# Performance work log

Hardware: AMD Instinct MI355X
Metric: run time of the kernel (lower is better)

The kernel has to match this reference:

```python
import jax, jax.numpy as jnp
import numpy as np

B, S, IN, HID, NH, HD, R, WIN, TK = 2, 2048, 64, 512, 8, 64, 64, 5, 16
C1, C2, C3 = 171, 171, 170  # hidden_dim split across 3 conv branches (512 = 171+171+170)


def _conv(xc, w, b, pad):
    y = jax.lax.conv_general_dilated(xc, w, window_strides=(1,), padding=[(pad, pad)],
                                     dimension_numbers=('NCH', 'OIH', 'NCH'))
    return jax.nn.relu(y + b[None, :, None])


def setup_inputs():
    key = jax.random.key(0)
    ks = jax.random.split(key, 22)
    p = lambda k, sh: jax.random.normal(k, sh, jnp.float32) * 0.05
    return {
        'x': jax.random.normal(ks[0], (B, S, IN), jnp.float32),
        'conv1_w': p(ks[1], (C1, IN, 3)), 'conv1_b': p(ks[2], (C1,)),
        'conv2_w': p(ks[3], (C2, IN, 5)), 'conv2_b': p(ks[4], (C2,)),
        'conv3_w': p(ks[5], (C3, IN, 7)), 'conv3_b': p(ks[6], (C3,)),
        'Wq': p(ks[7], (HID, HID)), 'bq': p(ks[8], (HID,)),
        'Wk': p(ks[9], (HID, HID)), 'bk': p(ks[10], (HID,)),
        'Wv': p(ks[11], (HID, HID)), 'bv': p(ks[12], (HID,)),
        'Wkp': p(ks[13], (R, HD)), 'bkp': p(ks[14], (R,)),
        'Wvp': p(ks[15], (R, HD)), 'bvp': p(ks[16], (R,)),
        'Wo': p(ks[17], (HID, HID)), 'bo': p(ks[18], (HID,)),
        'ln_g': jnp.ones((HID,), jnp.float32), 'ln_b': jnp.zeros((HID,), jnp.float32),
    }


def reference(x, conv1_w, conv1_b, conv2_w, conv2_b, conv3_w, conv3_b,
              Wq, bq, Wk, bk, Wv, bv, Wkp, bkp, Wvp, bvp, Wo, bo, ln_g, ln_b):
    # multi-scale conv front-end
    xc = x.transpose(0, 2, 1)  # [B, IN, S]
    h = jnp.concatenate([_conv(xc, conv1_w, conv1_b, 1),
                         _conv(xc, conv2_w, conv2_b, 2),
                         _conv(xc, conv3_w, conv3_b, 3)], axis=1).transpose(0, 2, 1)  # [B,S,HID]

    def heads(W_, b_):
        return (h @ W_.T + b_).reshape(B, S, NH, HD).transpose(0, 2, 1, 3)  # [B,NH,S,HD]

    Q, K, V = heads(Wq, bq), heads(Wk, bk), heads(Wv, bv)
    Kp = K @ Wkp.T + bkp  # [B,NH,S,R]
    Vp = V @ Wvp.T + bvp

    # local sliding-window attention; -inf masking reproduces the per-t boundary slicing
    hw = WIN // 2
    idx = jnp.arange(S)[:, None] + jnp.arange(-hw, hw + 1)[None, :]
    valid = (idx >= 0) & (idx < S)
    idxc = jnp.clip(idx, 0, S - 1)
    Kw = K[:, :, idxc, :]
    Vw = V[:, :, idxc, :]
    ls = jnp.einsum('bhsd,bhswd->bhsw', Q, Kw) / jnp.sqrt(jnp.float32(HD))
    ls = jnp.where(valid[None, None], ls, -jnp.inf)
    local = jnp.einsum('bhsw,bhswd->bhsd', jax.nn.softmax(ls, axis=-1), Vw)

    # top-k low-rank global attention (HD == R required by original einsum)
    gs = jnp.einsum('bhqd,bhkd->bhqk', Q, Kp) / jnp.sqrt(jnp.float32(R))  # [B,NH,S,S]
    tv, ti = jax.lax.top_k(gs, TK)
    tw = jax.nn.softmax(tv, axis=-1)  # [B,NH,S,TK]
    bi = jnp.arange(B)[:, None, None, None]
    hi = jnp.arange(NH)[None, :, None, None]
    topV = Vp[bi, hi, ti]  # [B,NH,S,TK,R]
    sp = jnp.einsum('bhqk,bhqkr->bhqr', tw, topV)
    sp = sp @ Wvp.T + bvp  # extra value_proj applied to sparse output, as in original

    out = ((local + sp) * 0.5).transpose(0, 2, 1, 3).reshape(B, S, HID)
    out = out @ Wo.T + bo
    res = out + h
    mu = res.mean(-1, keepdims=True)
    var = ((res - mu) ** 2).mean(-1, keepdims=True)
    return (res - mu) / jnp.sqrt(var + 1e-5) * ln_g + ln_b
```

## Files before the change

### kernel.cpp

```cpp
#include <hip/hip_runtime.h>
#include <hip/hip_bf16.h>

#define BB 2
#define SS 2048
#define INC 64
#define HIDN 512
#define NHH 8
#define HDD 64
#define SP 2054

typedef __attribute__((ext_vector_type(8))) short bf16x8;
typedef __attribute__((ext_vector_type(4))) float f32x4;

__device__ __forceinline__ short f2bf(float f) {
  union { __hip_bfloat16 h; short s; } u;
  u.h = __float2bfloat16(f);
  return u.s;
}
__device__ __forceinline__ float bf2f(short s) {
  return __uint_as_float(((unsigned)(unsigned short)s) << 16);
}


__global__ __launch_bounds__(256) void prep_kernel(
    const float* __restrict__ x, const float* __restrict__ w1,
    const float* __restrict__ b1, const float* __restrict__ w2,
    const float* __restrict__ b2, const float* __restrict__ w3,
    const float* __restrict__ b3, const float* __restrict__ Wq,
    const float* __restrict__ Wk_, const float* __restrict__ Wv_,
    const float* __restrict__ bq, const float* __restrict__ bk_,
    const float* __restrict__ bv_, const float* __restrict__ Wo,
    const float* __restrict__ Wkp, const float* __restrict__ Wvp,
    const float* __restrict__ bvp, short* __restrict__ Wallbf,
    float* __restrict__ ball, short* __restrict__ Wobf,
    short* __restrict__ Wkpbf, short* __restrict__ W2bf,
    float* __restrict__ cvec, short* __restrict__ xbfp,
    short* __restrict__ Wcbf, float* __restrict__ bcat) {
  int i0 = blockIdx.x * 256 + threadIdx.x;
  int stride = gridDim.x * 256;
  for (int g = i0; g < 98304; g += stride) {
    int n = g >> 6;
    int k = (g & 63) << 3;
    const float* src;
    if (n < 512)       src = Wq  + (size_t)n * 512 + k;
    else if (n < 1024) src = Wk_ + (size_t)(n - 512) * 512 + k;
    else               src = Wv_ + (size_t)(n - 1024) * 512 + k;
    float4 f0 = *(const float4*)src;
    float4 f1 = *(const float4*)(src + 4);
    bf16x8 v;
    v[0] = f2bf(f0.x); v[1] = f2bf(f0.y); v[2] = f2bf(f0.z); v[3] = f2bf(f0.w);
    v[4] = f2bf(f1.x); v[5] = f2bf(f1.y); v[6] = f2bf(f1.z); v[7] = f2bf(f1.w);
    size_t off = (size_t)(n >> 6) * 32768 + (size_t)(k >> 5) * 2048 +
                 (size_t)((n & 63) >> 4) * 512 +
                 ((((k & 31) >> 3) * 16 + (n & 15)) << 3);
    *(bf16x8*)(Wallbf + off) = v;
  }
  for (int g = i0; g < 32768; g += stride) {
    int n = g >> 6;
    int k = (g & 63) << 3;
    const float* src = Wo + (size_t)n * 512 + k;
    float4 f0 = *(const float4*)src;
    float4 f1 = *(const float4*)(src + 4);
    bf16x8 v;
    v[0] = f2bf(f0.x); v[1] = f2bf(f0.y); v[2] = f2bf(f0.z); v[3] = f2bf(f0.w);
    v[4] = f2bf(f1.x); v[5] = f2bf(f1.y); v[6] = f2bf(f1.z); v[7] = f2bf(f1.w);
    size_t off = (size_t)(n >> 6) * 32768 + (size_t)(k >> 5) * 2048 +
                 (size_t)((n & 63) >> 4) * 512 +
                 ((((k & 31) >> 3) * 16 + (n & 15)) << 3);
    *(bf16x8*)(Wobf + off) = v;
  }
  for (int g = i0; g < BB * SP * 8; g += stride) {
    int row = g >> 3, c0 = (g & 7) << 3;
    int b = row / SP, pr = row - b * SP;
    int sg = pr - 3;
    bf16x8 v;
    if (sg >= 0 && sg < SS) {
      const float* src = x + ((size_t)(b * SS + sg) << 6) + c0;
      float4 f0 = *(const float4*)src;
      float4 f1 = *(const float4*)(src + 4);
      v[0] = f2bf(f0.x); v[1] = f2bf(f0.y); v[2] = f2bf(f0.z); v[3] = f2bf(f0.w);
      v[4] = f2bf(f1.x); v[5] = f2bf(f1.y); v[6] = f2bf(f1.z); v[7] = f2bf(f1.w);
    } else {
#pragma unroll
      for (int e = 0; e < 8; e++) v[e] = 0;
    }
    *(bf16x8*)(xbfp + ((size_t)row << 3 << 3) + c0) = v;
  }
  for (int g = i0; g < 28672; g += stride) {
    int c = g / 56;
    int rem = g - c * 56;
    int k = rem << 3;
    int t = k >> 6;
    int ci0 = k & 63;
    bf16x8 v;
#pragma unroll
    for (int e = 0; e < 8; e++) {
      int ci = ci0 + e;
      float val = 0.f;
      if (c < 171) {
        int kk = t - 2;
        if (kk >= 0 && kk < 3) val = w1[(c * 64 + ci) * 3 + kk];
      } else if (c < 342) {
        int kk = t - 1;
        if (kk >= 0 && kk < 5) val = w2[((c - 171) * 64 + ci) * 5 + kk];
      } else {
        val = w3[((c - 342) * 64 + ci) * 7 + t];
      }
      v[e] = f2bf(val);
    }
    size_t off = (size_t)(c >> 6) * 28672 + (size_t)(k >> 5) * 2048 +
                 (size_t)((c & 63) >> 4) * 512 +
                 ((((k & 31) >> 3) * 16 + (c & 15)) << 3);
    *(bf16x8*)(Wcbf + off) = v;
  }
  for (int idx = i0; idx < 4096; idx += stride) {
    Wkpbf[idx] = f2bf(Wkp[idx]);
    int j = idx >> 6, d = idx & 63;
    float s = 0.f;
#pragma unroll 8
    for (int i = 0; i < 64; i++) s += Wvp[j * 64 + i] * Wvp[i * 64 + d];
    W2bf[idx] = f2bf(s);
  }
  if (i0 < 1536) {
    float v;
    if (i0 < 512)       v = bq[i0];
    else if (i0 < 1024) v = bk_[i0 - 512];
    else                v = bv_[i0 - 1024];
    ball[i0] = v;
  }
  if (i0 < 512) {
    float v;
    if (i0 < 171)      v = b1[i0];
    else if (i0 < 342) v = b2[i0 - 171];
    else               v = b3[i0 - 342];
    bcat[i0] = v;
  }
  if (i0 < 64) {
    float s = bvp[i0];
#pragma unroll 8
    for (int i = 0; i < 64; i++) s += bvp[i] * Wvp[i0 * 64 + i];
    cvec[i0] = s;
  }
}

__global__ __launch_bounds__(256, 4) void gemm_conv(
    const short* __restrict__ xbfp, const short* __restrict__ Wcbf,
    const float* __restrict__ bcat, short* __restrict__ hbf) {
  int m0 = blockIdx.x * 128;
  int n0 = blockIdx.y * 64;
  int tid = threadIdx.x;
  int wvv = tid >> 6, lane = tid & 63;
  int quad = lane >> 4, l16 = lane & 15;
  int mw = m0 + wvv * 32;
  int r0 = mw + l16, r1 = r0 + 16;
  int b0 = r0 >> 11, s0 = r0 & 2047;
  int b1 = r1 >> 11, s1 = r1 & 2047;
  const short* ap0 = xbfp + (size_t)(b0 * SP + s0) * 64 + quad * 8;
  const short* ap1 = xbfp + (size_t)(b1 * SP + s1) * 64 + quad * 8;
  const short* bp = Wcbf + (size_t)(n0 >> 6) * 28672 + lane * 8;
  f32x4 acc[2][4] = {};
  bf16x8 cA0 = *(const bf16x8*)ap0;
  bf16x8 cA1 = *(const bf16x8*)ap1;
  bf16x8 cB0 = *(const bf16x8*)(bp + 0 * 512);
  bf16x8 cB1 = *(const bf16x8*)(bp + 1 * 512);
  bf16x8 cB2 = *(const bf16x8*)(bp + 2 * 512);
  bf16x8 cB3 = *(const bf16x8*)(bp + 3 * 512);
#pragma unroll 2
  for (int ks = 0; ks < 14; ks++) {
    int kn = (ks + 1 < 14 ? ks + 1 : 13);
    int offa = kn * 32;
    int offb = kn * 2048;
    bf16x8 nA0 = *(const bf16x8*)(ap0 + offa);
    bf16x8 nA1 = *(const bf16x8*)(ap1 + offa);
    bf16x8 nB0 = *(const bf16x8*)(bp + offb + 0 * 512);
    bf16x8 nB1 = *(const bf16x8*)(bp + offb + 1 * 512);
    bf16x8 nB2 = *(const bf16x8*)(bp + offb + 2 * 512);
    bf16x8 nB3 = *(const bf16x8*)(bp + offb + 3 * 512);
    acc[0][0] = __builtin_amdgcn_mfma_f32_16x16x32_bf16(cA0, cB0, acc[0][0], 0, 0, 0);
    acc[1][0] = __builtin_amdgcn_mfma_f32_16x16x32_bf16(cA1, cB0, acc[1][0], 0, 0, 0);
    acc[0][1] = __builtin_amdgcn_mfma_f32_16x16x32_bf16(cA0, cB1, acc[0][1], 0, 0, 0);
    acc[1][1] = __builtin_amdgcn_mfma_f32_16x16x32_bf16(cA1, cB1, acc[1][1], 0, 0, 0);
    acc[0][2] = __builtin_amdgcn_mfma_f32_16x16x32_bf16(cA0, cB2, acc[0][2], 0, 0, 0);
    acc[1][2] = __builtin_amdgcn_mfma_f32_16x16x32_bf16(cA1, cB2, acc[1][2], 0, 0, 0);
    acc[0][3] = __builtin_amdgcn_mfma_f32_16x16x32_bf16(cA0, cB3, acc[0][3], 0, 0, 0);
    acc[1][3] = __builtin_amdgcn_mfma_f32_16x16x32_bf16(cA1, cB3, acc[1][3], 0, 0, 0);
    cA0 = nA0; cA1 = nA1;
    cB0 = nB0; cB1 = nB1; cB2 = nB2; cB3 = nB3;
  }
#pragma unroll
  for (int mt = 0; mt < 2; mt++) {
#pragma unroll
    for (int r = 0; r < 4; r++) {
      int m = mw + mt * 16 + quad * 4 + r;
#pragma unroll
      for (int t = 0; t < 4; t++) {
        int n = n0 + t * 16 + l16;
        float v = fmaxf(acc[mt][t][r] + bcat[n], 0.f);
        hbf[(size_t)m * 512 + n] = f2bf(v);
      }
    }
  }
}

__global__ __launch_bounds__(256, 4) void gemm_qkv(
    const short* __restrict__ Abf, const short* __restrict__ Wbf,
    const float* __restrict__ bias, short* __restrict__ Qh,
    short* __restrict__ Kh, short* __restrict__ Vh) {
  int m0 = blockIdx.x * 128;
  int n0 = blockIdx.y * 64;
  int tid = threadIdx.x;
  int wvv = tid >> 6, lane = tid & 63;
  int quad = lane >> 4, l16 = lane & 15;
  int mw = m0 + wvv * 32;
  const short* ap0 = Abf + (size_t)(mw + l16) * 512 + quad * 8;
  const short* ap1 = ap0 + 16 * 512;
  const short* bp = Wbf + (size_t)(n0 >> 6) * 32768 + lane * 8;
  f32x4 acc[2][4] = {};
  bf16x8 cA0 = *(const bf16x8*)ap0;
  bf16x8 cA1 = *(const bf16x8*)ap1;
  bf16x8 cB0 = *(const bf16x8*)(bp + 0 * 512);
  bf16x8 cB1 = *(const bf16x8*)(bp + 1 * 512);
  bf16x8 cB2 = *(const bf16x8*)(bp + 2 * 512);
  bf16x8 cB3 = *(const bf16x8*)(bp + 3 * 512);
#pragma unroll 2
  for (int ks = 0; ks < 16; ks++) {
    int kn = (ks + 1 < 16 ? ks + 1 : 15);
    int offa = kn * 32;
    int offb = kn * 2048;
    bf16x8 nA0 = *(const bf16x8*)(ap0 + offa);
    bf16x8 nA1 = *(const bf16x8*)(ap1 + offa);
    bf16x8 nB0 = *(const bf16x8*)(bp + offb + 0 * 512);
    bf16x8 nB1 = *(const bf16x8*)(bp + offb + 1 * 512);
    bf16x8 nB2 = *(const bf16x8*)(bp + offb + 2 * 512);
    bf16x8 nB3 = *(const bf16x8*)(bp + offb + 3 * 512);
    acc[0][0] = __builtin_amdgcn_mfma_f32_16x16x32_bf16(cA0, cB0, acc[0][0], 0, 0, 0);
    acc[1][0] = __builtin_amdgcn_mfma_f32_16x16x32_bf16(cA1, cB0, acc[1][0], 0, 0, 0);
    acc[0][1] = __builtin_amdgcn_mfma_f32_16x16x32_bf16(cA0, cB1, acc[0][1], 0, 0, 0);
    acc[1][1] = __builtin_amdgcn_mfma_f32_16x16x32_bf16(cA1, cB1, acc[1][1], 0, 0, 0);
    acc[0][2] = __builtin_amdgcn_mfma_f32_16x16x32_bf16(cA0, cB2, acc[0][2], 0, 0, 0);
    acc[1][2] = __builtin_amdgcn_mfma_f32_16x16x32_bf16(cA1, cB2, acc[1][2], 0, 0, 0);
    acc[0][3] = __builtin_amdgcn_mfma_f32_16x16x32_bf16(cA0, cB3, acc[0][3], 0, 0, 0);
    acc[1][3] = __builtin_amdgcn_mfma_f32_16x16x32_bf16(cA1, cB3, acc[1][3], 0, 0, 0);
    cA0 = nA0; cA1 = nA1;
    cB0 = nB0; cB1 = nB1; cB2 = nB2; cB3 = nB3;
  }
  int which = n0 >> 9;
  int head = (n0 >> 6) & 7;
  short* dst = which == 0 ? Qh : (which == 1 ? Kh : Vh);
  float scale = which == 0 ? 0.125f : 1.0f;
#pragma unroll
  for (int mt = 0; mt < 2; mt++) {
#pragma unroll
    for (int r = 0; r < 4; r++) {
      int m = mw + mt * 16 + quad * 4 + r;
      int bb = m >> 11, s = m & 2047;
      size_t rowoff = ((size_t)(bb * 8 + head) * 2048 + s) * 64;
#pragma unroll
      for (int t = 0; t < 4; t++) {
        int hd = t * 16 + l16;
        float v = acc[mt][t][r] + bias[n0 + hd];
        dst[rowoff + hd] = f2bf(v * scale);
      }
    }
  }
}

__global__ __launch_bounds__(256, 4) void kpvp_local_kernel(
    const short* __restrict__ Kh, const short* __restrict__ Vh,
    const short* __restrict__ Wkpbf, const float* __restrict__ bkp,
    const short* __restrict__ W2bf, const float* __restrict__ cvec,
    short* __restrict__ Kfrag, float* __restrict__ Vpp,
    const short* __restrict__ Qh, float* __restrict__ ctxl) {
  int tid = threadIdx.x;
  __shared__ float Sloc[4][2][16][17];
  __shared__ float wloc[4][16][8];
  if (blockIdx.x < 256) {
    int m0 = blockIdx.x * 128;
    int wvv = tid >> 6, lane = tid & 63;
    int quad = lane >> 4, l16 = lane & 15;
    int mw = m0 + wvv * 32;
    {
      const short* ap0 = Kh + (size_t)(mw + l16) * 64 + quad * 8;
      const short* ap1 = ap0 + 16 * 64;
      const short* bp = Wkpbf + l16 * 64 + quad * 8;
      bf16x8 A00 = *(const bf16x8*)ap0, A01 = *(const bf16x8*)(ap0 + 32);
      bf16x8 A10 = *(const bf16x8*)ap1, A11 = *(const bf16x8*)(ap1 + 32);
      f32x4 acc[2][4] = {};
#pragma unroll
      for (int t = 0; t < 4; t++) {
        bf16x8 B0 = *(const bf16x8*)(bp + t * 16 * 64);
        bf16x8 B1 = *(const bf16x8*)(bp + t * 16 * 64 + 32);
        acc[0][t] = __builtin_amdgcn_mfma_f32_16x16x32_bf16(A00, B0, acc[0][t], 0, 0, 0);
        acc[0][t] = __builtin_amdgcn_mfma_f32_16x16x32_bf16(A01, B1, acc[0][t], 0, 0, 0);
        acc[1][t] = __builtin_amdgcn_mfma_f32_16x16x32_bf16(A10, B0, acc[1][t], 0, 0, 0);
        acc[1][t] = __builtin_amdgcn_mfma_f32_16x16x32_bf16(A11, B1, acc[1][t], 0, 0, 0);
      }
#pragma unroll
      for (int mt = 0; mt < 2; mt++)
#pragma unroll
        for (int r = 0; r < 4; r++) {
          int m = mw + mt * 16 + quad * 4 + r;
          int m15 = m & 15;
          size_t gbase = (size_t)(m >> 4) * 1024;
#pragma unroll
          for (int t = 0; t < 4; t++) {
            int n = t * 16 + l16;
            short val = f2bf(acc[mt][t][r] + bkp[n]);
            Kfrag[gbase + (size_t)(n >> 5) * 512 +
                  ((((n & 31) >> 3) * 16 + m15) << 3) + (n & 7)] = val;
          }
        }
    }
    {
      const short* ap0 = Vh + (size_t)(mw + l16) * 64 + quad * 8;
      const short* ap1 = ap0 + 16 * 64;
      const short* bp = W2bf + l16 * 64 + quad * 8;
      bf16x8 A00 = *(const bf16x8*)ap0, A01 = *(const bf16x8*)(ap0 + 32);
      bf16x8 A10 = *(const bf16x8*)ap1, A11 = *(const bf16x8*)(ap1 + 32);
      f32x4 acc[2][4] = {};
#pragma unroll
      for (int t = 0; t < 4; t++) {
        bf16x8 B0 = *(const bf16x8*)(bp + t * 16 * 64);
        bf16x8 B1 = *(const bf16x8*)(bp + t * 16 * 64 + 32);
        acc[0][t] = __builtin_amdgcn_mfma_f32_16x16x32_bf16(A00, B0, acc[0][t], 0, 0, 0);
        acc[0][t] = __builtin_amdgcn_mfma_f32_16x16x32_bf16(A01, B1, acc[0][t], 0, 0, 0);
        acc[1][t] = __builtin_amdgcn_mfma_f32_16x16x32_bf16(A10, B0, acc[1][t], 0, 0, 0);
        acc[1][t] = __builtin_amdgcn_mfma_f32_16x16x32_bf16(A11, B1, acc[1][t], 0, 0, 0);
      }
#pragma unroll
      for (int mt = 0; mt < 2; mt++)
#pragma unroll
        for (int r = 0; r < 4; r++) {
          int m = mw + mt * 16 + quad * 4 + r;
#pragma unroll
          for (int t = 0; t < 4; t++) {
            int n = t * 16 + l16;
            Vpp[(size_t)m * 64 + n] = acc[mt][t][r] + cvec[n];
          }
        }
    }
    return;
  }
  int wv = tid >> 6;
  int tile = (blockIdx.x - 256) * 4 + wv;
  int bh = tile >> 7;
  int q0 = (tile & 127) * 16;
  int lane = tid & 63;
  int quad = lane >> 4, l16 = lane & 15;

  const short* qbase = Qh + (size_t)(bh * 2048 + q0 + l16) * 64 + quad * 8;
  bf16x8 a0 = *(const bf16x8*)qbase;
  bf16x8 a1 = *(const bf16x8*)(qbase + 32);

  int k0a = min(max(q0 - 2 + l16, 0), 2047);
  int k1a = min(q0 + 6 + l16, 2047);
  const short* kb0 = Kh + (size_t)(bh * 2048 + k0a) * 64 + quad * 8;
  const short* kb1 = Kh + (size_t)(bh * 2048 + k1a) * 64 + quad * 8;
  bf16x8 B00 = *(const bf16x8*)kb0;
  bf16x8 B01 = *(const bf16x8*)(kb0 + 32);
  bf16x8 B10 = *(const bf16x8*)kb1;
  bf16x8 B11 = *(const bf16x8*)(kb1 + 32);
  f32x4 C0 = {0.f, 0.f, 0.f, 0.f};
  f32x4 C1 = {0.f, 0.f, 0.f, 0.f};
  C0 = __builtin_amdgcn_mfma_f32_16x16x32_bf16(a0, B00, C0, 0, 0, 0);
  C0 = __builtin_amdgcn_mfma_f32_16x16x32_bf16(a1, B01, C0, 0, 0, 0);
  C1 = __builtin_amdgcn_mfma_f32_16x16x32_bf16(a0, B10, C1, 0, 0, 0);
  C1 = __builtin_amdgcn_mfma_f32_16x16x32_bf16(a1, B11, C1, 0, 0, 0);
#pragma unroll
  for (int r = 0; r < 4; r++) {
    Sloc[wv][0][quad * 4 + r][l16] = C0[r];
    Sloc[wv][1][quad * 4 + r][l16] = C1[r];
  }
  __builtin_amdgcn_wave_barrier();
  if (lane < 16) {
    int q = lane;
    float sc[5];
    bool ok[5];
#pragma unroll
    for (int j = 0; j < 5; j++) {
      int offq = q + j - 2;
      int sg = q0 + offq;
      ok[j] = (sg >= 0 && sg < SS);
      int t = offq <= 13 ? 0 : 1;
      int col = t ? offq - 6 : offq + 2;
      sc[j] = ok[j] ? Sloc[wv][t][q][col] : -3.0e38f;
    }
    float m = -3.0e38f;
#pragma unroll
    for (int j = 0; j < 5; j++) m = fmaxf(m, sc[j]);
    float e[5], l = 0.f;
#pragma unroll
    for (int j = 0; j < 5; j++) {
      e[j] = ok[j] ? __expf(sc[j] - m) : 0.f;
      l += e[j];
    }
    float inv = 1.f / l;
#pragma unroll
    for (int j = 0; j < 5; j++) wloc[wv][q][j] = e[j] * inv;
  }
  __builtin_amdgcn_wave_barrier();
  {
    int q = lane >> 2, jb = (lane & 3) * 16;
    int s = q0 + q;
    float acc[16] = {};
#pragma unroll
    for (int j = 0; j < 5; j++) {
      int sg = s + j - 2;
      if (sg >= 0 && sg < SS) {
        float w = wloc[wv][q][j];
        const short* vr = Vh + (size_t)(bh * 2048 + sg) * 64 + jb;
#pragma unroll
        for (int u = 0; u < 16; u += 4) {
          short4 v4 = *(const short4*)(vr + u);
          acc[u + 0] += w * bf2f(v4.x);
          acc[u + 1] += w * bf2f(v4.y);
          acc[u + 2] += w * bf2f(v4.z);
          acc[u + 3] += w * bf2f(v4.w);
        }
      }
    }
    float* orow = ctxl + (size_t)(bh * 2048 + s) * 64 + jb;
#pragma unroll
    for (int u = 0; u < 16; u += 4)
      *(float4*)(orow + u) =
          make_float4(acc[u], acc[u + 1], acc[u + 2], acc[u + 3]);
  }
}

__global__ __launch_bounds__(256, 4) void global_attn(
    const short* __restrict__ Qh, const short* __restrict__ Kfrag,
    const float* __restrict__ Vpp, const float* __restrict__ ctxl,
    short* __restrict__ ctxcb) {
  int tid = threadIdx.x;
  int wv = tid >> 6;
  int lane = tid & 63;
  int quad = lane >> 4, l16 = lane & 15;
  int tb = wv >> 1;
  int half = wv & 1;
  int p = blockIdx.x;
  int bh = (p & 7) * 2 + ((p >> 3) & 1);
  int seg = p >> 4;
  int tile = seg * 2 + tb;
  int q0 = tile * 16;

  __shared__ unsigned swl[4][16][17];
  __shared__ float twl[2][16][17];
  __shared__ int   txl[2][16][17];

  const short* qbase = Qh + (size_t)(bh * 2048 + q0 + l16) * 64 + quad * 8;
  bf16x8 a0 = *(const bf16x8*)qbase;
  bf16x8 a1 = *(const bf16x8*)(qbase + 32);

  const short* kf =
      Kfrag + (size_t)bh * (128 * 1024) + (size_t)half * (64 * 1024) + lane * 8;

  unsigned er[4][8];
#pragma unroll
  for (int a = 0; a < 4; a++)
#pragma unroll
    for (int j = 0; j < 8; j++) er[a][j] = 0u;

  auto insert8 = [&](unsigned (&e)[8], unsigned cand) {
    unsigned n0, n1, n2, n3, n4, n5, n6, n7;
    asm("v_max_u32 %0, %1, %2" : "=v"(n0) : "v"(e[0]), "v"(cand));
    asm("v_med3_u32 %0, %1, %2, %3" : "=v"(n1) : "v"(e[0]), "v"(e[1]), "v"(cand));
    asm("v_med3_u32 %0, %1, %2, %3" : "=v"(n2) : "v"(e[1]), "v"(e[2]), "v"(cand));
    asm("v_med3_u32 %0, %1, %2, %3" : "=v"(n3) : "v"(e[2]), "v"(e[3]), "v"(cand));
    asm("v_med3_u32 %0, %1, %2, %3" : "=v"(n4) : "v"(e[3]), "v"(e[4]), "v"(cand));
    asm("v_med3_u32 %0, %1, %2, %3" : "=v"(n5) : "v"(e[4]), "v"(e[5]), "v"(cand));
    asm("v_med3_u32 %0, %1, %2, %3" : "=v"(n6) : "v"(e[5]), "v"(e[6]), "v"(cand));
    asm("v_med3_u32 %0, %1, %2, %3" : "=v"(n7) : "v"(e[6]), "v"(e[7]), "v"(cand));
    e[0] = n0; e[1] = n1; e[2] = n2; e[3] = n3;
    e[4] = n4; e[5] = n5; e[6] = n6; e[7] = n7;
  };
  auto mkcand = [&](float s, int idxr) -> unsigned {
    unsigned u = __float_as_uint(s);
    u ^= ((unsigned)((int)u >> 31)) | 0x80000000u;
    return (u & 0xFFFFF800u) | (unsigned)idxr;
  };

  int idxb = 2047 - half * 1024 - l16;
#pragma unroll 4
  for (int g = 0; g < 64; g++) {
    bf16x8 B00 = *(const bf16x8*)(kf + g * 1024);
    bf16x8 B01 = *(const bf16x8*)(kf + g * 1024 + 512);
    f32x4 C0 = {0.f, 0.f, 0.f, 0.f};
    C0 = __builtin_amdgcn_mfma_f32_16x16x32_bf16(a0, B00, C0, 0, 0, 0);
    C0 = __builtin_amdgcn_mfma_f32_16x16x32_bf16(a1, B01, C0, 0, 0, 0);
    int idxr = idxb - (g << 4);
    insert8(er[0], mkcand(C0[0], idxr));
    insert8(er[1], mkcand(C0[1], idxr));
    insert8(er[2], mkcand(C0[2], idxr));
    insert8(er[3], mkcand(C0[3], idxr));
  }

  {
    unsigned sw[4] = {0u, 0u, 0u, 0u};
#pragma unroll
    for (int t = 0; t < 16; t++) {
#pragma unroll
      for (int a = 0; a < 4; a++) {
        unsigned w = er[a][0];
#pragma unroll
        for (int mm = 1; mm <= 8; mm <<= 1) {
          unsigned o = (unsigned)__shfl_xor((int)w, mm);
          w = w > o ? w : o;
        }
        bool pop = (er[a][0] == w);
#pragma unroll
        for (int j = 0; j < 7; j++) er[a][j] = pop ? er[a][j + 1] : er[a][j];
        er[a][7] = pop ? 0u : er[a][7];
        if (l16 == t) sw[a] = w;
      }
    }
#pragma unroll
    for (int a = 0; a < 4; a++) swl[wv][quad * 4 + a][l16] = sw[a];
  }
  __syncthreads();

  if (tid < 32) {
    int tb2 = tid >> 4, q = tid & 15;
    const unsigned* A = swl[tb2 * 2][q];
    const unsigned* Bv = swl[tb2 * 2 + 1][q];
    auto decode = [&](unsigned w) -> float {
      unsigned wb = w & 0xFFFFF800u;
      unsigned uu = (w & 0x80000000u) ? (wb ^ 0x80000000u) : ~wb;
      return (w == 0u) ? -1.0e30f : __uint_as_float(uu);
    };
    unsigned h0 = A[0], h1 = Bv[0];
    float mval = decode(h0 > h1 ? h0 : h1);
    float lsum = 0.f;
    float ev[16];
    int ki[16];
#pragma unroll
    for (int i = 0; i < 16; i++) {
      unsigned wa = A[i], wb2 = Bv[15 - i];
      unsigned w = wa > wb2 ? wa : wb2;
      float sv = decode(w);
      float ex = __expf(sv - mval);
      lsum += ex;
      ev[i] = ex;
      ki[i] = 2047 - (int)(w & 0x7FFu);
    }
    float inv = 1.f / lsum;
#pragma unroll
    for (int i = 0; i < 16; i++) {
      twl[tb2][q][i] = ev[i] * inv;
      txl[tb2][q][i] = ki[i];
    }
  }
  __syncthreads();

  {
    int tb2 = tid >> 7;
    int r = tid & 127;
    int q = r >> 3, d0 = (r & 7) * 8;
    int tile2 = seg * 2 + tb2;
    int q02 = tile2 * 16;
    int b = bh >> 3, hh = bh & 7;
    const float* vball = Vpp + (size_t)bh * (2048 * 64) + d0;
    float acc[8];
#pragma unroll
    for (int u = 0; u < 8; u++) acc[u] = 0.f;
#pragma unroll 4
    for (int j = 0; j < 16; j++) {
      float w = twl[tb2][q][j];
      const float* vr = vball + (size_t)txl[tb2][q][j] * 64;
      float4 v0 = *(const float4*)vr;
      float4 v1 = *(const float4*)(vr + 4);
      acc[0] += w * v0.x; acc[1] += w * v0.y;
      acc[2] += w * v0.z; acc[3] += w * v0.w;
      acc[4] += w * v1.x; acc[5] += w * v1.y;
      acc[6] += w * v1.z; acc[7] += w * v1.w;
    }
    int s = q02 + q;
    const float* lrow = ctxl + (size_t)(bh * 2048 + s) * 64 + d0;
    short* orow = ctxcb + (size_t)(b * 2048 + s) * 512 + hh * 64 + d0;
    float4 lv0 = *(const float4*)lrow;
    float4 lv1 = *(const float4*)(lrow + 4);
    short4 o0, o1;
    o0.x = f2bf(0.5f * (lv0.x + acc[0]));
    o0.y = f2bf(0.5f * (lv0.y + acc[1]));
    o0.z = f2bf(0.5f * (lv0.z + acc[2]));
    o0.w = f2bf(0.5f * (lv0.w + acc[3]));
    o1.x = f2bf(0.5f * (lv1.x + acc[4]));
    o1.y = f2bf(0.5f * (lv1.y + acc[5]));
    o1.z = f2bf(0.5f * (lv1.z + acc[6]));
    o1.w = f2bf(0.5f * (lv1.w + acc[7]));
    *(short4*)orow = o0;
    *(short4*)(orow + 4) = o1;
  }
}

__global__ __launch_bounds__(256, 4) void gemm_wo(
    const short* __restrict__ Abf, const short* __restrict__ Wbf,
    const float* __restrict__ bo, const short* __restrict__ hbf,
    float* __restrict__ outp) {
  int m0 = blockIdx.x * 128;
  int n0 = blockIdx.y * 64;
  int tid = threadIdx.x;
  int wvv = tid >> 6, lane = tid & 63;
  int quad = lane >> 4, l16 = lane & 15;
  int mw = m0 + wvv * 32;
  const short* ap0 = Abf + (size_t)(mw + l16) * 512 + quad * 8;
  const short* ap1 = ap0 + 16 * 512;
  const short* bp = Wbf + (size_t)(n0 >> 6) * 32768 + lane * 8;
  f32x4 acc[2][4] = {};
  bf16x8 cA0 = *(const bf16x8*)ap0;
  bf16x8 cA1 = *(const bf16x8*)ap1;
  bf16x8 cB0 = *(const bf16x8*)(bp + 0 * 512);
  bf16x8 cB1 = *(const bf16x8*)(bp + 1 * 512);
  bf16x8 cB2 = *(const bf16x8*)(bp + 2 * 512);
  bf16x8 cB3 = *(const bf16x8*)(bp + 3 * 512);
#pragma unroll 2
  for (int ks = 0; ks < 16; ks++) {
    int kn = (ks + 1 < 16 ? ks + 1 : 15);
    int offa = kn * 32;
    int offb = kn * 2048;
    bf16x8 nA0 = *(const bf16x8*)(ap0 + offa);
    bf16x8 nA1 = *(const bf16x8*)(ap1 + offa);
    bf16x8 nB0 = *(const bf16x8*)(bp + offb + 0 * 512);
    bf16x8 nB1 = *(const bf16x8*)(bp + offb + 1 * 512);
    bf16x8 nB2 = *(const bf16x8*)(bp + offb + 2 * 512);
    bf16x8 nB3 = *(const bf16x8*)(bp + offb + 3 * 512);
    acc[0][0] = __builtin_amdgcn_mfma_f32_16x16x32_bf16(cA0, cB0, acc[0][0], 0, 0, 0);
    acc[1][0] = __builtin_amdgcn_mfma_f32_16x16x32_bf16(cA1, cB0, acc[1][0], 0, 0, 0);
    acc[0][1] = __builtin_amdgcn_mfma_f32_16x16x32_bf16(cA0, cB1, acc[0][1], 0, 0, 0);
    acc[1][1] = __builtin_amdgcn_mfma_f32_16x16x32_bf16(cA1, cB1, acc[1][1], 0, 0, 0);
    acc[0][2] = __builtin_amdgcn_mfma_f32_16x16x32_bf16(cA0, cB2, acc[0][2], 0, 0, 0);
    acc[1][2] = __builtin_amdgcn_mfma_f32_16x16x32_bf16(cA1, cB2, acc[1][2], 0, 0, 0);
    acc[0][3] = __builtin_amdgcn_mfma_f32_16x16x32_bf16(cA0, cB3, acc[0][3], 0, 0, 0);
    acc[1][3] = __builtin_amdgcn_mfma_f32_16x16x32_bf16(cA1, cB3, acc[1][3], 0, 0, 0);
    cA0 = nA0; cA1 = nA1;
    cB0 = nB0; cB1 = nB1; cB2 = nB2; cB3 = nB3;
  }
#pragma unroll
  for (int mt = 0; mt < 2; mt++) {
#pragma unroll
    for (int r = 0; r < 4; r++) {
      int m = mw + mt * 16 + quad * 4 + r;
#pragma unroll
      for (int t = 0; t < 4; t++) {
        int n = n0 + t * 16 + l16;
        outp[(size_t)m * 512 + n] =
            acc[mt][t][r] + bo[n] + bf2f(hbf[(size_t)m * 512 + n]);
      }
    }
  }
}

__global__ __launch_bounds__(256) void ln_kernel(float* __restrict__ o,
                                                 const float* __restrict__ g,
                                                 const float* __restrict__ bb) {
  int row = blockIdx.x;
  int tid = threadIdx.x;
  float v0 = o[row * 512 + tid];
  float v1 = o[row * 512 + 256 + tid];
  float s = v0 + v1;
  float s2 = v0 * v0 + v1 * v1;
#pragma unroll
  for (int off = 1; off < 64; off <<= 1) {
    s += __shfl_xor(s, off);
    s2 += __shfl_xor(s2, off);
  }
  __shared__ float ps[4], ps2[4];
  int w = tid >> 6;
  if ((tid & 63) == 0) { ps[w] = s; ps2[w] = s2; }
  __syncthreads();
  float S = ps[0] + ps[1] + ps[2] + ps[3];
  float S2 = ps2[0] + ps2[1] + ps2[2] + ps2[3];
  float mu = S * (1.f / 512.f);
  float var = S2 * (1.f / 512.f) - mu * mu;
  float inv = rsqrtf(var + 1e-5f);
  o[row * 512 + tid] = (v0 - mu) * inv * g[tid] + bb[tid];
  o[row * 512 + 256 + tid] = (v1 - mu) * inv * g[tid + 256] + bb[tid + 256];
}

extern "C" void kernel_launch(void* const* d_in, const int* in_sizes, int n_in,
                              void* d_out, int out_size, void* d_ws,
                              size_t ws_size, hipStream_t stream) {
  const float* x   = (const float*)d_in[0];
  const float* w1  = (const float*)d_in[1];
  const float* b1  = (const float*)d_in[2];
  const float* w2  = (const float*)d_in[3];
  const float* b2  = (const float*)d_in[4];
  const float* w3  = (const float*)d_in[5];
  const float* b3  = (const float*)d_in[6];
  const float* Wq  = (const float*)d_in[7];
  const float* bq  = (const float*)d_in[8];
  const float* Wk  = (const float*)d_in[9];
  const float* bk  = (const float*)d_in[10];
  const float* Wv  = (const float*)d_in[11];
  const float* bv  = (const float*)d_in[12];
  const float* Wkp = (const float*)d_in[13];
  const float* bkp = (const float*)d_in[14];
  const float* Wvp = (const float*)d_in[15];
  const float* bvp = (const float*)d_in[16];
  const float* Wo  = (const float*)d_in[17];
  const float* bo  = (const float*)d_in[18];
  const float* lng = (const float*)d_in[19];
  const float* lnb = (const float*)d_in[20];

  float* p = (float*)d_ws;
  short* Wallbf = (short*)p;  p += 786432;
  float* ball   = p;          p += 2048;
  short* Wobf   = (short*)p;  p += 262144;
  short* Wkpbf  = (short*)p;  p += 4096;
  short* W2bf   = (short*)p;  p += 4096;
  float* cvec   = p;          p += 64;
  short* xbfp   = (short*)p;  p += 262912;
  short* Wcbf   = (short*)p;  p += 229376;
  float* bcat   = p;          p += 512;
  short* hbf    = (short*)p;  p += 1048576;
  short* Qh     = (short*)p;  p += 1048576;
  short* Kh     = (short*)p;  p += 1048576;
  short* Vh     = (short*)p;  p += 1048576;
  short* Kfrag  = (short*)p;  p += 1048576;
  float* Vpp    = p;          p += 2097152;
  float* ctxl   = p;          p += 2097152;
  short* ctxcb  = (short*)p;  p += 1048576;
  float* outF   = (float*)d_out;

  prep_kernel<<<512, 256, 0, stream>>>(x, w1, b1, w2, b2, w3, b3, Wq, Wk, Wv,
                                       bq, bk, bv, Wo, Wkp, Wvp, bvp, Wallbf,
                                       ball, Wobf, Wkpbf, W2bf, cvec, xbfp,
                                       Wcbf, bcat);
  {
    dim3 g(32, 8);
    gemm_conv<<<g, 256, 0, stream>>>(xbfp, Wcbf, bcat, hbf);
  }
  {
    dim3 g(32, 24);
    gemm_qkv<<<g, 256, 0, stream>>>(hbf, Wallbf, ball, Qh, Kh, Vh);
  }
  kpvp_local_kernel<<<768, 256, 0, stream>>>(Kh, Vh, Wkpbf, bkp, W2bf, cvec,
                                             Kfrag, Vpp, Qh, ctxl);
  global_attn<<<1024, 256, 0, stream>>>(Qh, Kfrag, Vpp, ctxl, ctxcb);
  {
    dim3 g(32, 8);
    gemm_wo<<<g, 256, 0, stream>>>(ctxcb, Wobf, bo, hbf, outF);
  }
  ln_kernel<<<4096, 256, 0, stream>>>(outF, lng, lnb);
}
```

Baseline: 230.2 us.

## Store GEMM A operands in MFMA fragment-packed layout for coalesced loads

The conv GEMM now writes a second copy of h in a fragment-packed layout, and the global-attention epilogue writes its context output in that same packed layout. The QKV and Wo GEMMs then read A operands as contiguous per-lane 16-byte chunks, replacing the earlier strided row-major loads. The aim is better-coalesced A-operand fetches in the two 512-K GEMMs. The cost is an extra scattered 2-byte store per element in the conv epilogue, an extra buffer, and more scattered writes in the attention epilogue.

```diff
diff --git a/kernel.cpp b/kernel.cpp
--- a/kernel.cpp
+++ b/kernel.cpp
@@ -84,7 +84,7 @@
 #pragma unroll
       for (int e = 0; e < 8; e++) v[e] = 0;
     }
-    *(bf16x8*)(xbfp + ((size_t)row << 3 << 3) + c0) = v;
+    *(bf16x8*)(xbfp + ((size_t)row << 6) + c0) = v;
   }
   for (int g = i0; g < 28672; g += stride) {
     int c = g / 56;
@@ -145,7 +145,8 @@
 
 __global__ __launch_bounds__(256, 4) void gemm_conv(
     const short* __restrict__ xbfp, const short* __restrict__ Wcbf,
-    const float* __restrict__ bcat, short* __restrict__ hbf) {
+    const float* __restrict__ bcat, short* __restrict__ hbf,
+    short* __restrict__ hAf) {
   int m0 = blockIdx.x * 128;
   int n0 = blockIdx.y * 64;
   int tid = threadIdx.x;
@@ -192,18 +193,23 @@
 #pragma unroll
     for (int r = 0; r < 4; r++) {
       int m = mw + mt * 16 + quad * 4 + r;
+      size_t abase = (size_t)(m >> 4) * 8192;
+      int m15 = m & 15;
 #pragma unroll
       for (int t = 0; t < 4; t++) {
         int n = n0 + t * 16 + l16;
         float v = fmaxf(acc[mt][t][r] + bcat[n], 0.f);
-        hbf[(size_t)m * 512 + n] = f2bf(v);
+        short val = f2bf(v);
+        hbf[(size_t)m * 512 + n] = val;
+        hAf[abase + (size_t)(n >> 5) * 512 +
+            ((((n & 31) >> 3) * 16 + m15) << 3) + (n & 7)] = val;
       }
     }
   }
 }
 
 __global__ __launch_bounds__(256, 4) void gemm_qkv(
-    const short* __restrict__ Abf, const short* __restrict__ Wbf,
+    const short* __restrict__ hAf, const short* __restrict__ Wbf,
     const float* __restrict__ bias, short* __restrict__ Qh,
     short* __restrict__ Kh, short* __restrict__ Vh) {
   int m0 = blockIdx.x * 128;
@@ -212,8 +218,8 @@
   int wvv = tid >> 6, lane = tid & 63;
   int quad = lane >> 4, l16 = lane & 15;
   int mw = m0 + wvv * 32;
-  const short* ap0 = Abf + (size_t)(mw + l16) * 512 + quad * 8;
-  const short* ap1 = ap0 + 16 * 512;
+  const short* ap0 = hAf + (size_t)(mw >> 4) * 8192 + lane * 8;
+  const short* ap1 = ap0 + 8192;
   const short* bp = Wbf + (size_t)(n0 >> 6) * 32768 + lane * 8;
   f32x4 acc[2][4] = {};
   bf16x8 cA0 = *(const bf16x8*)ap0;
@@ -225,10 +231,10 @@
 #pragma unroll 2
   for (int ks = 0; ks < 16; ks++) {
     int kn = (ks + 1 < 16 ? ks + 1 : 15);
-    int offa = kn * 32;
+    int offab = kn * 512;
     int offb = kn * 2048;
-    bf16x8 nA0 = *(const bf16x8*)(ap0 + offa);
-    bf16x8 nA1 = *(const bf16x8*)(ap1 + offa);
+    bf16x8 nA0 = *(const bf16x8*)(ap0 + offab);
+    bf16x8 nA1 = *(const bf16x8*)(ap1 + offab);
     bf16x8 nB0 = *(const bf16x8*)(bp + offb + 0 * 512);
     bf16x8 nB1 = *(const bf16x8*)(bp + offb + 1 * 512);
     bf16x8 nB2 = *(const bf16x8*)(bp + offb + 2 * 512);
@@ -575,7 +581,10 @@
     }
     int s = q02 + q;
     const float* lrow = ctxl + (size_t)(bh * 2048 + s) * 64 + d0;
-    short* orow = ctxcb + (size_t)(b * 2048 + s) * 512 + hh * 64 + d0;
+    int M = b * 2048 + s;
+    int k = hh * 64 + d0;
+    size_t aoff = (size_t)(M >> 4) * 8192 + (size_t)(k >> 5) * 512 +
+                  ((((k & 31) >> 3) * 16 + (M & 15)) << 3);
     float4 lv0 = *(const float4*)lrow;
     float4 lv1 = *(const float4*)(lrow + 4);
     short4 o0, o1;
@@ -587,8 +596,8 @@
     o1.y = f2bf(0.5f * (lv1.y + acc[5]));
     o1.z = f2bf(0.5f * (lv1.z + acc[6]));
     o1.w = f2bf(0.5f * (lv1.w + acc[7]));
-    *(short4*)orow = o0;
-    *(short4*)(orow + 4) = o1;
+    *(short4*)(ctxcb + aoff) = o0;
+    *(short4*)(ctxcb + aoff + 4) = o1;
   }
 }
 
@@ -602,8 +611,8 @@
   int wvv = tid >> 6, lane = tid & 63;
   int quad = lane >> 4, l16 = lane & 15;
   int mw = m0 + wvv * 32;
-  const short* ap0 = Abf + (size_t)(mw + l16) * 512 + quad * 8;
-  const short* ap1 = ap0 + 16 * 512;
+  const short* ap0 = Abf + (size_t)(mw >> 4) * 8192 + lane * 8;
+  const short* ap1 = ap0 + 8192;
   const short* bp = Wbf + (size_t)(n0 >> 6) * 32768 + lane * 8;
   f32x4 acc[2][4] = {};
   bf16x8 cA0 = *(const bf16x8*)ap0;
@@ -615,10 +624,10 @@
 #pragma unroll 2
   for (int ks = 0; ks < 16; ks++) {
     int kn = (ks + 1 < 16 ? ks + 1 : 15);
-    int offa = kn * 32;
+    int offab = kn * 512;
     int offb = kn * 2048;
-    bf16x8 nA0 = *(const bf16x8*)(ap0 + offa);
-    bf16x8 nA1 = *(const bf16x8*)(ap1 + offa);
+    bf16x8 nA0 = *(const bf16x8*)(ap0 + offab);
+    bf16x8 nA1 = *(const bf16x8*)(ap1 + offab);
     bf16x8 nB0 = *(const bf16x8*)(bp + offb + 0 * 512);
     bf16x8 nB1 = *(const bf16x8*)(bp + offb + 1 * 512);
     bf16x8 nB2 = *(const bf16x8*)(bp + offb + 2 * 512);
@@ -712,6 +721,7 @@
   short* Wcbf   = (short*)p;  p += 229376;
   float* bcat   = p;          p += 512;
   short* hbf    = (short*)p;  p += 1048576;
+  short* hAf    = (short*)p;  p += 1048576;
   short* Qh     = (short*)p;  p += 1048576;
   short* Kh     = (short*)p;  p += 1048576;
   short* Vh     = (short*)p;  p += 1048576;
@@ -727,11 +737,11 @@
                                        Wcbf, bcat);
   {
     dim3 g(32, 8);
-    gemm_conv<<<g, 256, 0, stream>>>(xbfp, Wcbf, bcat, hbf);
+    gemm_conv<<<g, 256, 0, stream>>>(xbfp, Wcbf, bcat, hbf, hAf);
   }
   {
     dim3 g(32, 24);
-    gemm_qkv<<<g, 256, 0, stream>>>(hbf, Wallbf, ball, Qh, Kh, Vh);
+    gemm_qkv<<<g, 256, 0, stream>>>(hAf, Wallbf, ball, Qh, Kh, Vh);
   }
   kpvp_local_kernel<<<768, 256, 0, stream>>>(Kh, Vh, Wkpbf, bkp, W2bf, cvec,
                                              Kfrag, Vpp, Qh, ctxl);
```

New measurement: 222.5 us. 1.03x faster.
